# Optimization experiments

Measured on AMD Instinct MI355X. Metric: run time of the kernel, lower is better.

The kernel has to match this reference:

```python
import jax, jax.numpy as jnp
import numpy as np

SEQ, BATCH, IN_DIM, HID, OUT_DIM = 2048, 128, 128, 256, 64


def setup_inputs() -> dict:
    key = jax.random.key(0)
    ks = jax.random.split(key, 7)
    s = 1.0 / np.sqrt(HID)
    x = jax.random.normal(ks[0], (SEQ, BATCH, IN_DIM), dtype=jnp.float32)
    W_ih = jax.random.uniform(ks[1], (4 * HID, IN_DIM), minval=-s, maxval=s, dtype=jnp.float32)
    W_hh = jax.random.uniform(ks[2], (4 * HID, HID), minval=-s, maxval=s, dtype=jnp.float32)
    b_ih = jax.random.uniform(ks[3], (4 * HID,), minval=-s, maxval=s, dtype=jnp.float32)
    b_hh = jax.random.uniform(ks[4], (4 * HID,), minval=-s, maxval=s, dtype=jnp.float32)
    W_out = jax.random.uniform(ks[5], (OUT_DIM, HID), minval=-s, maxval=s, dtype=jnp.float32)
    b_out = jax.random.uniform(ks[6], (OUT_DIM,), minval=-s, maxval=s, dtype=jnp.float32)
    return {"x": x, "W_ih": W_ih, "W_hh": W_hh, "b_ih": b_ih, "b_hh": b_hh,
            "W_out": W_out, "b_out": b_out}


def _lstm(x, W_ih, W_hh, b_ih, b_hh):
    # Precompute input contribution for all timesteps: [T, B, 4H]
    xg = jnp.einsum('tbi,gi->tbg', x, W_ih) + b_ih + b_hh
    H = W_hh.shape[1]
    B = x.shape[1]
    h0 = jnp.zeros((B, H), dtype=x.dtype)
    c0 = jnp.zeros((B, H), dtype=x.dtype)

    def step(carry, xg_t):
        h, c = carry
        gates = xg_t + h @ W_hh.T  # [B, 4H]
        i, f, g, o = jnp.split(gates, 4, axis=-1)  # PyTorch gate order i,f,g,o
        i = jax.nn.sigmoid(i)
        f = jax.nn.sigmoid(f)
        g = jnp.tanh(g)
        o = jax.nn.sigmoid(o)
        c_new = f * c + i * g
        h_new = o * jnp.tanh(c_new)
        return (h_new, c_new), h_new

    _, r_out = jax.lax.scan(step, (h0, c0), xg)  # r_out: [T, B, H]
    return r_out


def reference(x, W_ih, W_hh, b_ih, b_hh, W_out, b_out):
    r_out = _lstm(x, W_ih, W_hh, b_ih, b_hh)
    out = jnp.einsum('tbh,oh->tbo', r_out, W_out) + b_out  # [T, B, OUT]
    return out
```

## Files before the change

### kernel.cpp

```cpp
#include <hip/hip_runtime.h>
#include <stdint.h>


#define T_SEQ 2048
#define BATCH 128
#define IN_D  128
#define HID   256
#define OUTD  64

typedef _Float16 half2_t __attribute__((ext_vector_type(2)));

__device__ __forceinline__ float dot2f(uint32_t w, uint32_t h, float acc) {
#if __has_builtin(__builtin_amdgcn_fdot2)
  return __builtin_amdgcn_fdot2(__builtin_bit_cast(half2_t, w),
                                __builtin_bit_cast(half2_t, h), acc, false);
#else
  half2_t a = __builtin_bit_cast(half2_t, w);
  half2_t b = __builtin_bit_cast(half2_t, h);
  return acc + (float)a[0] * (float)b[0] + (float)a[1] * (float)b[1];
#endif
}

__device__ __forceinline__ uint32_t pack2(float a, float b) {
  union { _Float16 h[2]; uint32_t u; } u_;
  u_.h[0] = (_Float16)a; u_.h[1] = (_Float16)b;
  return u_.u;
}

__device__ __forceinline__ uint64_t ld64_ag(const uint64_t* p) {
  return __hip_atomic_load(p, __ATOMIC_RELAXED, __HIP_MEMORY_SCOPE_AGENT);
}
__device__ __forceinline__ void st64_ag(uint64_t* p, uint64_t v) {
  __hip_atomic_store(p, v, __ATOMIC_RELAXED, __HIP_MEMORY_SCOPE_AGENT);
}

#define BARRIER() do {                                   \
  asm volatile("s_waitcnt lgkmcnt(0)" ::: "memory");     \
  __builtin_amdgcn_s_barrier();                          \
  asm volatile("" ::: "memory");                         \
} while (0)

__device__ __forceinline__ uint4 load8(const float* __restrict__ Wih,
                                       const float* __restrict__ Whh,
                                       int row, int k) {
  const float* p0 = (k     < IN_D) ? (Wih + (size_t)row * IN_D + k)
                                   : (Whh + (size_t)row * HID + (k - IN_D));
  const float* p1 = (k + 4 < IN_D) ? (Wih + (size_t)row * IN_D + k + 4)
                                   : (Whh + (size_t)row * HID + (k + 4 - IN_D));
  const float4 a = *(const float4*)p0;
  const float4 b = *(const float4*)p1;
  uint4 r;
  r.x = pack2(a.x, a.y); r.y = pack2(a.z, a.w);
  r.z = pack2(b.x, b.y); r.w = pack2(b.z, b.w);
  return r;
}

__device__ __forceinline__ float sigm(float v) { return 1.f / (1.f + __expf(-v)); }
__device__ __forceinline__ float tanhx(float v) {
  float a = fabsf(v);
  float e = __expf(2.f * a);
  float r = 1.f - 2.f / (e + 1.f);
  return v < 0.f ? -r : r;
}

#define DOT_U(g, u, A)                      \
  A = dot2f(W##g##_##u.x, hv0_.x, A);       \
  A = dot2f(W##g##_##u.y, hv0_.y, A);       \
  A = dot2f(W##g##_##u.z, hv0_.z, A);       \
  A = dot2f(W##g##_##u.w, hv0_.w, A);

#define DOT_G(g, A)                                            \
  { const uint4 hv0_ = hp[0]; DOT_U(g, 0, A) }                 \
  { const uint4 hv0_ = hp[1]; DOT_U(g, 1, A) }                 \
  { const uint4 hv0_ = hp[2]; DOT_U(g, 2, A) }                 \
  { const uint4 hv0_ = hp[3]; DOT_U(g, 3, A) }                 \
  { const uint4 hv0_ = hp[4]; DOT_U(g, 4, A) }                 \
  { const uint4 hv0_ = hp[5]; DOT_U(g, 5, A) }

#define PIN4(v) asm volatile("" : "+v"(v.x), "+v"(v.y), "+v"(v.z), "+v"(v.w));

__global__ __launch_bounds__(512, 2)
void lstm_persist(const float* __restrict__ x,   const float* __restrict__ Wih,
                  const float* __restrict__ Whh, const float* __restrict__ bih,
                  const float* __restrict__ bhh, const float* __restrict__ Wout,
                  const float* __restrict__ bout_g, float* __restrict__ out,
                  uint64_t* exch)
{
  __shared__ alignas(16) uint32_t hx[2 * 192];

  const int tid = threadIdx.x;
  const int w   = blockIdx.x;
  const int p   = w & 63;
  const int q   = w >> 6;
  const int jj  = tid >> 3;
  const int ks  = tid & 7;
  const int rbase = (q << 6) + jj;
  const int kb    = ks * 48;

  uint4 W0_0, W0_1, W0_2, W0_3, W0_4, W0_5;
  uint4 W1_0, W1_1, W1_2, W1_3, W1_4, W1_5;
  uint4 W2_0, W2_1, W2_2, W2_3, W2_4, W2_5;
  uint4 W3_0, W3_1, W3_2, W3_3, W3_4, W3_5;
#define LOADG(g)                                             \
  { const int row = (g) * HID + rbase;                       \
    W##g##_0 = load8(Wih, Whh, row, kb +  0);                \
    W##g##_1 = load8(Wih, Whh, row, kb +  8);                \
    W##g##_2 = load8(Wih, Whh, row, kb + 16);                \
    W##g##_3 = load8(Wih, Whh, row, kb + 24);                \
    W##g##_4 = load8(Wih, Whh, row, kb + 32);                \
    W##g##_5 = load8(Wih, Whh, row, kb + 40); }
  LOADG(0) LOADG(1) LOADG(2) LOADG(3)
#undef LOADG
  PIN4(W0_0) PIN4(W0_1) PIN4(W0_2) PIN4(W0_3) PIN4(W0_4) PIN4(W0_5)
  PIN4(W1_0) PIN4(W1_1) PIN4(W1_2) PIN4(W1_3) PIN4(W1_4) PIN4(W1_5)
  PIN4(W2_0) PIN4(W2_1) PIN4(W2_2) PIN4(W2_3) PIN4(W2_4) PIN4(W2_5)
  PIN4(W3_0) PIN4(W3_1) PIN4(W3_2) PIN4(W3_3) PIN4(W3_4) PIN4(W3_5)

  float b0 = bih[0 * HID + rbase] + bhh[0 * HID + rbase];
  float b1 = bih[1 * HID + rbase] + bhh[1 * HID + rbase];
  float b2 = bih[2 * HID + rbase] + bhh[2 * HID + rbase];
  float b3 = bih[3 * HID + rbase] + bhh[3 * HID + rbase];

  const int oo = tid >> 5, orow = (tid >> 4) & 1, os = tid & 15;
  uint4 woA, woB;
  {
    const float* wo = Wout + (size_t)((q << 4) + oo) * HID + (os << 4);
    const float4 v0 = *(const float4*)(wo + 0), v1 = *(const float4*)(wo + 4);
    const float4 v2 = *(const float4*)(wo + 8), v3 = *(const float4*)(wo + 12);
    woA.x = pack2(v0.x, v0.y); woA.y = pack2(v0.z, v0.w);
    woA.z = pack2(v1.x, v1.y); woA.w = pack2(v1.z, v1.w);
    woB.x = pack2(v2.x, v2.y); woB.y = pack2(v2.z, v2.w);
    woB.z = pack2(v3.x, v3.y); woB.w = pack2(v3.z, v3.w);
  }
  PIN4(woA) PIN4(woB)
  const float bo = bout_g[(q << 4) + oo];

  if (tid < 256) hx[(tid >> 7) * 192 + 64 + (tid & 127)] = 0u;
  if (tid < 128) {
    const int row = tid >> 6, cc = tid & 63;
    const float2 xv = *(const float2*)(x + ((size_t)(2 * p + row)) * IN_D + 2 * cc);
    hx[row * 192 + cc] = pack2(xv.x, xv.y);
  }
  float c = 0.f;
  __syncthreads();

  const int pi  = tid - 64;
  const int pqq = pi >> 6, pl = pi & 63;
  const int pqp = pqq + (pqq >= q);
  const int pws = (pqp << 6) | p;

  for (int t = 0; t <= T_SEQ; ++t) {
    uint32_t xn = 0;
    uint32_t packed = 0;
    uint64_t polled = 0;
    if (t < T_SEQ) {
      if (tid >= 256 && tid < 384 && (t + 1) < T_SEQ) {
        const int row = (tid - 256) >> 6, cc = (tid - 256) & 63;
        const float2 xv = *(const float2*)(x + (size_t)(t + 1) * BATCH * IN_D +
                                           (size_t)(2 * p + row) * IN_D + 2 * cc);
        xn = pack2(xv.x, xv.y);
      }
      float a00 = 0.f, a10 = 0.f, a20 = 0.f, a30 = 0.f;
      float a01 = 0.f, a11 = 0.f, a21 = 0.f, a31 = 0.f;
      {
        const uint4* hp = (const uint4*)hx + ks * 6;
        DOT_G(0, a00) DOT_G(1, a10) DOT_G(2, a20) DOT_G(3, a30)
      }
      {
        const uint4* hp = (const uint4*)hx + 48 + ks * 6;
        DOT_G(0, a01) DOT_G(1, a11) DOT_G(2, a21) DOT_G(3, a31)
      }
      float u0, u1, u2, u3;
      {
        const int r = ks & 1;
        float t0, t1;
        t0 = a00 + __shfl_xor(a00, 1, 64); t1 = a01 + __shfl_xor(a01, 1, 64);
        u0 = r ? t1 : t0;
        t0 = a10 + __shfl_xor(a10, 1, 64); t1 = a11 + __shfl_xor(a11, 1, 64);
        u1 = r ? t1 : t0;
        t0 = a20 + __shfl_xor(a20, 1, 64); t1 = a21 + __shfl_xor(a21, 1, 64);
        u2 = r ? t1 : t0;
        t0 = a30 + __shfl_xor(a30, 1, 64); t1 = a31 + __shfl_xor(a31, 1, 64);
        u3 = r ? t1 : t0;
      }
      u0 += __shfl_xor(u0, 2, 64); u0 += __shfl_xor(u0, 4, 64);
      u1 += __shfl_xor(u1, 2, 64); u1 += __shfl_xor(u1, 4, 64);
      u2 += __shfl_xor(u2, 2, 64); u2 += __shfl_xor(u2, 4, 64);
      u3 += __shfl_xor(u3, 2, 64); u3 += __shfl_xor(u3, 4, 64);
      if (ks < 2) {
        const int r = ks;
        const float iv = sigm(b0 + u0), fv = sigm(b1 + u1);
        const float gv = tanhx(b2 + u2), ov = sigm(b3 + u3);
        c = fv * c + iv * gv;
        const float hn = ov * tanhx(c);
        union { _Float16 h; unsigned short u; } cv; cv.h = (_Float16)hn;
        const uint32_t mine  = cv.u;
        const uint32_t other = (uint32_t)(unsigned short)__shfl_xor((int)mine, 8, 64);
        if (!(jj & 1)) {
          packed = mine | (other << 16);
          const uint64_t entry = ((uint64_t)(uint32_t)(t + 1) << 32) | packed;
          st64_ag(exch + (((size_t)w << 7) | ((t & 1) << 6)) + (r << 5) + (jj >> 1),
                  entry);
        }
      }
    }
    if (t >= 1) {
      const uint4* hq = (const uint4*)hx + orow * 48 + 16 + os * 2;
      const uint4 h0 = hq[0], h1 = hq[1];
      float oa = 0.f;
      oa = dot2f(woA.x, h0.x, oa); oa = dot2f(woA.y, h0.y, oa);
      oa = dot2f(woA.z, h0.z, oa); oa = dot2f(woA.w, h0.w, oa);
      oa = dot2f(woB.x, h1.x, oa); oa = dot2f(woB.y, h1.y, oa);
      oa = dot2f(woB.z, h1.z, oa); oa = dot2f(woB.w, h1.w, oa);
      oa += __shfl_xor(oa, 1, 64); oa += __shfl_xor(oa, 2, 64);
      oa += __shfl_xor(oa, 4, 64); oa += __shfl_xor(oa, 8, 64);
      if (os == 0)
        out[((size_t)(t - 1) * BATCH + 2 * p + orow) * OUTD + (q << 4) + oo] = oa + bo;
    }
    if (t < T_SEQ && tid >= 64 && tid < 256) {
      const uint64_t* src = exch + (((size_t)pws << 7) | ((t & 1) << 6)) + pl;
      const uint32_t want = (uint32_t)(t + 1);
      do { polled = ld64_ag(src); } while ((uint32_t)(polled >> 32) != want);
    }
    BARRIER();
    if (t < T_SEQ) {
      if (ks < 2 && !(jj & 1))
        hx[ks * 192 + 64 + (q << 5) + (jj >> 1)] = packed;
      if (tid >= 256 && tid < 384 && (t + 1) < T_SEQ)
        hx[((tid - 256) >> 6) * 192 + ((tid - 256) & 63)] = xn;
      if (tid >= 64 && tid < 256)
        hx[(pl >> 5) * 192 + 64 + (pqp << 5) + (pl & 31)] = (uint32_t)polled;
    }
    BARRIER();
  }
}

extern "C" void kernel_launch(void* const* d_in, const int* in_sizes, int n_in,
                              void* d_out, int out_size, void* d_ws, size_t ws_size,
                              hipStream_t stream) {
  (void)in_sizes; (void)n_in; (void)out_size; (void)ws_size;
  const float* x    = (const float*)d_in[0];
  const float* Wih  = (const float*)d_in[1];
  const float* Whh  = (const float*)d_in[2];
  const float* bih  = (const float*)d_in[3];
  const float* bhh  = (const float*)d_in[4];
  const float* Wout = (const float*)d_in[5];
  const float* bout = (const float*)d_in[6];
  float* out = (float*)d_out;

  uint64_t* exch = (uint64_t*)d_ws;

  hipLaunchKernelGGL(lstm_persist, dim3(256), dim3(512), 0, stream,
                     x, Wih, Whh, bih, bhh, Wout, bout, out, exch);
}
```

Measured before the change: 5.616 ms.

## Split input projection off the recurrent path and overlap it with the exchange poll

The gate weights are split into separate W_hh and W_ih register tiles. The x contribution for step t+1 is now computed between the two block barriers, in the same window where threads spin-wait on the cross-block h exchange, so the dependent h·W_hh dot shrinks from 384 to 256 inputs per step. To make this possible, x is prefetched two steps ahead into a double-buffered LDS ring. The cost is extra registers for the partial sums, and the poll now sits after the XG work, which could lengthen the spin window on some threads.

```diff
diff --git a/kernel.cpp b/kernel.cpp
--- a/kernel.cpp
+++ b/kernel.cpp
@@ -34,21 +34,9 @@
   __hip_atomic_store(p, v, __ATOMIC_RELAXED, __HIP_MEMORY_SCOPE_AGENT);
 }
 
-#define BARRIER() do {                                   \
-  asm volatile("s_waitcnt lgkmcnt(0)" ::: "memory");     \
-  __builtin_amdgcn_s_barrier();                          \
-  asm volatile("" ::: "memory");                         \
-} while (0)
-
-__device__ __forceinline__ uint4 load8(const float* __restrict__ Wih,
-                                       const float* __restrict__ Whh,
-                                       int row, int k) {
-  const float* p0 = (k     < IN_D) ? (Wih + (size_t)row * IN_D + k)
-                                   : (Whh + (size_t)row * HID + (k - IN_D));
-  const float* p1 = (k + 4 < IN_D) ? (Wih + (size_t)row * IN_D + k + 4)
-                                   : (Whh + (size_t)row * HID + (k + 4 - IN_D));
-  const float4 a = *(const float4*)p0;
-  const float4 b = *(const float4*)p1;
+__device__ __forceinline__ uint4 loadW8(const float* __restrict__ pw) {
+  const float4 a = *(const float4*)pw;
+  const float4 b = *(const float4*)(pw + 4);
   uint4 r;
   r.x = pack2(a.x, a.y); r.y = pack2(a.z, a.w);
   r.z = pack2(b.x, b.y); r.w = pack2(b.z, b.w);
@@ -63,21 +51,31 @@
   return v < 0.f ? -r : r;
 }
 
-#define DOT_U(g, u, A)                      \
-  A = dot2f(W##g##_##u.x, hv0_.x, A);       \
-  A = dot2f(W##g##_##u.y, hv0_.y, A);       \
-  A = dot2f(W##g##_##u.z, hv0_.z, A);       \
-  A = dot2f(W##g##_##u.w, hv0_.w, A);
-
-#define DOT_G(g, A)                                            \
-  { const uint4 hv0_ = hp[0]; DOT_U(g, 0, A) }                 \
-  { const uint4 hv0_ = hp[1]; DOT_U(g, 1, A) }                 \
-  { const uint4 hv0_ = hp[2]; DOT_U(g, 2, A) }                 \
-  { const uint4 hv0_ = hp[3]; DOT_U(g, 3, A) }                 \
-  { const uint4 hv0_ = hp[4]; DOT_U(g, 4, A) }                 \
-  { const uint4 hv0_ = hp[5]; DOT_U(g, 5, A) }
+#define D4(Wv, Hv, A)                       \
+  A = dot2f(Wv.x, Hv.x, A);                 \
+  A = dot2f(Wv.y, Hv.y, A);                 \
+  A = dot2f(Wv.z, Hv.z, A);                 \
+  A = dot2f(Wv.w, Hv.w, A);
 
 #define PIN4(v) asm volatile("" : "+v"(v.x), "+v"(v.y), "+v"(v.z), "+v"(v.w));
+
+#define XG_ALL(slotbase)                                                     \
+  {                                                                          \
+    const uint4* xp0 = (const uint4*)(xring + (slotbase)) + ks * 2;          \
+    const uint4* xp1 = (const uint4*)(xring + (slotbase) + 64) + ks * 2;     \
+    const uint4 xa = xp0[0], xb = xp0[1];                                    \
+    const uint4 xc = xp1[0], xd = xp1[1];                                    \
+    axg00 = 0.f; axg10 = 0.f; axg20 = 0.f; axg30 = 0.f;                      \
+    axg01 = 0.f; axg11 = 0.f; axg21 = 0.f; axg31 = 0.f;                      \
+    D4(X0_0, xa, axg00) D4(X0_1, xb, axg00)                                  \
+    D4(X1_0, xa, axg10) D4(X1_1, xb, axg10)                                  \
+    D4(X2_0, xa, axg20) D4(X2_1, xb, axg20)                                  \
+    D4(X3_0, xa, axg30) D4(X3_1, xb, axg30)                                  \
+    D4(X0_0, xc, axg01) D4(X0_1, xd, axg01)                                  \
+    D4(X1_0, xc, axg11) D4(X1_1, xd, axg11)                                  \
+    D4(X2_0, xc, axg21) D4(X2_1, xd, axg21)                                  \
+    D4(X3_0, xc, axg31) D4(X3_1, xd, axg31)                                  \
+  }
 
 __global__ __launch_bounds__(512, 2)
 void lstm_persist(const float* __restrict__ x,   const float* __restrict__ Wih,
@@ -86,7 +84,8 @@
                   const float* __restrict__ bout_g, float* __restrict__ out,
                   uint64_t* exch)
 {
-  __shared__ alignas(16) uint32_t hx[2 * 192];
+  __shared__ alignas(16) uint32_t hbuf[2 * 128];
+  __shared__ alignas(16) uint32_t xring[2 * 2 * 64];
 
   const int tid = threadIdx.x;
   const int w   = blockIdx.x;
@@ -95,26 +94,24 @@
   const int jj  = tid >> 3;
   const int ks  = tid & 7;
   const int rbase = (q << 6) + jj;
-  const int kb    = ks * 48;
-
-  uint4 W0_0, W0_1, W0_2, W0_3, W0_4, W0_5;
-  uint4 W1_0, W1_1, W1_2, W1_3, W1_4, W1_5;
-  uint4 W2_0, W2_1, W2_2, W2_3, W2_4, W2_5;
-  uint4 W3_0, W3_1, W3_2, W3_3, W3_4, W3_5;
-#define LOADG(g)                                             \
-  { const int row = (g) * HID + rbase;                       \
-    W##g##_0 = load8(Wih, Whh, row, kb +  0);                \
-    W##g##_1 = load8(Wih, Whh, row, kb +  8);                \
-    W##g##_2 = load8(Wih, Whh, row, kb + 16);                \
-    W##g##_3 = load8(Wih, Whh, row, kb + 24);                \
-    W##g##_4 = load8(Wih, Whh, row, kb + 32);                \
-    W##g##_5 = load8(Wih, Whh, row, kb + 40); }
+
+  uint4 H0_0, H0_1, H0_2, H0_3, X0_0, X0_1;
+  uint4 H1_0, H1_1, H1_2, H1_3, X1_0, X1_1;
+  uint4 H2_0, H2_1, H2_2, H2_3, X2_0, X2_1;
+  uint4 H3_0, H3_1, H3_2, H3_3, X3_0, X3_1;
+#define LOADG(g)                                                 \
+  { const int row = (g) * HID + rbase;                           \
+    const float* ph = Whh + (size_t)row * HID + (ks << 5);       \
+    H##g##_0 = loadW8(ph);      H##g##_1 = loadW8(ph + 8);       \
+    H##g##_2 = loadW8(ph + 16); H##g##_3 = loadW8(ph + 24);      \
+    const float* px = Wih + (size_t)row * IN_D + (ks << 4);      \
+    X##g##_0 = loadW8(px);      X##g##_1 = loadW8(px + 8); }
   LOADG(0) LOADG(1) LOADG(2) LOADG(3)
 #undef LOADG
-  PIN4(W0_0) PIN4(W0_1) PIN4(W0_2) PIN4(W0_3) PIN4(W0_4) PIN4(W0_5)
-  PIN4(W1_0) PIN4(W1_1) PIN4(W1_2) PIN4(W1_3) PIN4(W1_4) PIN4(W1_5)
-  PIN4(W2_0) PIN4(W2_1) PIN4(W2_2) PIN4(W2_3) PIN4(W2_4) PIN4(W2_5)
-  PIN4(W3_0) PIN4(W3_1) PIN4(W3_2) PIN4(W3_3) PIN4(W3_4) PIN4(W3_5)
+  PIN4(H0_0) PIN4(H0_1) PIN4(H0_2) PIN4(H0_3) PIN4(X0_0) PIN4(X0_1)
+  PIN4(H1_0) PIN4(H1_1) PIN4(H1_2) PIN4(H1_3) PIN4(X1_0) PIN4(X1_1)
+  PIN4(H2_0) PIN4(H2_1) PIN4(H2_2) PIN4(H2_3) PIN4(X2_0) PIN4(X2_1)
+  PIN4(H3_0) PIN4(H3_1) PIN4(H3_2) PIN4(H3_3) PIN4(X3_0) PIN4(X3_1)
 
   float b0 = bih[0 * HID + rbase] + bhh[0 * HID + rbase];
   float b1 = bih[1 * HID + rbase] + bhh[1 * HID + rbase];
@@ -135,11 +132,16 @@
   PIN4(woA) PIN4(woB)
   const float bo = bout_g[(q << 4) + oo];
 
-  if (tid < 256) hx[(tid >> 7) * 192 + 64 + (tid & 127)] = 0u;
+  if (tid < 256) hbuf[tid] = 0u;
   if (tid < 128) {
     const int row = tid >> 6, cc = tid & 63;
-    const float2 xv = *(const float2*)(x + ((size_t)(2 * p + row)) * IN_D + 2 * cc);
-    hx[row * 192 + cc] = pack2(xv.x, xv.y);
+    const float2 xv = *(const float2*)(x + (size_t)(2 * p + row) * IN_D + 2 * cc);
+    xring[row * 64 + cc] = pack2(xv.x, xv.y);
+  } else if (tid < 256) {
+    const int i = tid - 128, row = i >> 6, cc = i & 63;
+    const float2 xv = *(const float2*)(x + (size_t)BATCH * IN_D +
+                                       (size_t)(2 * p + row) * IN_D + 2 * cc);
+    xring[128 + row * 64 + cc] = pack2(xv.x, xv.y);
   }
   float c = 0.f;
   __syncthreads();
@@ -149,26 +151,36 @@
   const int pqp = pqq + (pqq >= q);
   const int pws = (pqp << 6) | p;
 
+  float axg00, axg10, axg20, axg30, axg01, axg11, axg21, axg31;
+  XG_ALL(0)
+
   for (int t = 0; t <= T_SEQ; ++t) {
     uint32_t xn = 0;
     uint32_t packed = 0;
-    uint64_t polled = 0;
     if (t < T_SEQ) {
-      if (tid >= 256 && tid < 384 && (t + 1) < T_SEQ) {
+      if (tid >= 256 && tid < 384 && (t + 2) < T_SEQ) {
         const int row = (tid - 256) >> 6, cc = (tid - 256) & 63;
-        const float2 xv = *(const float2*)(x + (size_t)(t + 1) * BATCH * IN_D +
+        const float2 xv = *(const float2*)(x + (size_t)(t + 2) * BATCH * IN_D +
                                            (size_t)(2 * p + row) * IN_D + 2 * cc);
         xn = pack2(xv.x, xv.y);
       }
-      float a00 = 0.f, a10 = 0.f, a20 = 0.f, a30 = 0.f;
-      float a01 = 0.f, a11 = 0.f, a21 = 0.f, a31 = 0.f;
+      float a00 = axg00, a10 = axg10, a20 = axg20, a30 = axg30;
+      float a01 = axg01, a11 = axg11, a21 = axg21, a31 = axg31;
       {
-        const uint4* hp = (const uint4*)hx + ks * 6;
-        DOT_G(0, a00) DOT_G(1, a10) DOT_G(2, a20) DOT_G(3, a30)
+        const uint4* hb = (const uint4*)hbuf + (ks << 2);
+        const uint4 h0 = hb[0], h1 = hb[1], h2 = hb[2], h3 = hb[3];
+        D4(H0_0, h0, a00) D4(H0_1, h1, a00) D4(H0_2, h2, a00) D4(H0_3, h3, a00)
+        D4(H1_0, h0, a10) D4(H1_1, h1, a10) D4(H1_2, h2, a10) D4(H1_3, h3, a10)
+        D4(H2_0, h0, a20) D4(H2_1, h1, a20) D4(H2_2, h2, a20) D4(H2_3, h3, a20)
+        D4(H3_0, h0, a30) D4(H3_1, h1, a30) D4(H3_2, h2, a30) D4(H3_3, h3, a30)
       }
       {
-        const uint4* hp = (const uint4*)hx + 48 + ks * 6;
-        DOT_G(0, a01) DOT_G(1, a11) DOT_G(2, a21) DOT_G(3, a31)
+        const uint4* hb = (const uint4*)hbuf + 32 + (ks << 2);
+        const uint4 h0 = hb[0], h1 = hb[1], h2 = hb[2], h3 = hb[3];
+        D4(H0_0, h0, a01) D4(H0_1, h1, a01) D4(H0_2, h2, a01) D4(H0_3, h3, a01)
+        D4(H1_0, h0, a11) D4(H1_1, h1, a11) D4(H1_2, h2, a11) D4(H1_3, h3, a11)
+        D4(H2_0, h0, a21) D4(H2_1, h1, a21) D4(H2_2, h2, a21) D4(H2_3, h3, a21)
+        D4(H3_0, h0, a31) D4(H3_1, h1, a31) D4(H3_2, h2, a31) D4(H3_3, h3, a31)
       }
       float u0, u1, u2, u3;
       {
@@ -205,7 +217,7 @@
       }
     }
     if (t >= 1) {
-      const uint4* hq = (const uint4*)hx + orow * 48 + 16 + os * 2;
+      const uint4* hq = (const uint4*)hbuf + orow * 32 + os * 2;
       const uint4 h0 = hq[0], h1 = hq[1];
       float oa = 0.f;
       oa = dot2f(woA.x, h0.x, oa); oa = dot2f(woA.y, h0.y, oa);
@@ -217,21 +229,23 @@
       if (os == 0)
         out[((size_t)(t - 1) * BATCH + 2 * p + orow) * OUTD + (q << 4) + oo] = oa + bo;
     }
-    if (t < T_SEQ && tid >= 64 && tid < 256) {
-      const uint64_t* src = exch + (((size_t)pws << 7) | ((t & 1) << 6)) + pl;
-      const uint32_t want = (uint32_t)(t + 1);
-      do { polled = ld64_ag(src); } while ((uint32_t)(polled >> 32) != want);
-    }
-    BARRIER();
+    __syncthreads();
     if (t < T_SEQ) {
       if (ks < 2 && !(jj & 1))
-        hx[ks * 192 + 64 + (q << 5) + (jj >> 1)] = packed;
-      if (tid >= 256 && tid < 384 && (t + 1) < T_SEQ)
-        hx[((tid - 256) >> 6) * 192 + ((tid - 256) & 63)] = xn;
-      if (tid >= 64 && tid < 256)
-        hx[(pl >> 5) * 192 + 64 + (pqp << 5) + (pl & 31)] = (uint32_t)polled;
+        hbuf[ks * 128 + (q << 5) + (jj >> 1)] = packed;
+      if (tid >= 256 && tid < 384 && (t + 2) < T_SEQ)
+        xring[((t & 1) << 7) + (((tid - 256) >> 6) << 6) + ((tid - 256) & 63)] = xn;
+      if (t + 1 < T_SEQ)
+        XG_ALL(((t + 1) & 1) << 7)
+      if (tid >= 64 && tid < 256) {
+        const uint64_t* src = exch + (((size_t)pws << 7) | ((t & 1) << 6)) + pl;
+        const uint32_t want = (uint32_t)(t + 1);
+        uint64_t e;
+        do { e = ld64_ag(src); } while ((uint32_t)(e >> 32) != want);
+        hbuf[(pl >> 5) * 128 + (pqp << 5) + (pl & 31)] = (uint32_t)e;
+      }
     }
-    BARRIER();
+    __syncthreads();
   }
 }
 
```

Result: faster. 4.912 ms (-12.5%).
